# Kernel tuning notes

Measured on AMD Instinct MI355X. Metric: run time of the kernel, lower is better.

The kernel has to match this reference:

```python
import jax, jax.numpy as jnp
import numpy as np

B, N, D, H = 8, 1024, 768, 12
HD = D // H  # 64


def setup_inputs() -> dict:
    key = jax.random.key(0)
    ks = jax.random.split(key, 10)
    input_graph = jax.random.normal(ks[0], (B, N, D), dtype=jnp.float32)
    u = jax.random.uniform(ks[1], (B, N, N), dtype=jnp.float32)
    keep = jax.random.uniform(ks[2], (B, N, N)) < 0.15
    adj = jnp.where(keep, u, 0.0)
    s = 1.0 / np.sqrt(D)
    Wq = jax.random.normal(ks[3], (D, D), dtype=jnp.float32) * s
    bq = jnp.zeros((D,), dtype=jnp.float32)
    Wk = jax.random.normal(ks[4], (D, D), dtype=jnp.float32) * s
    bk = jnp.zeros((D,), dtype=jnp.float32)
    Wv = jax.random.normal(ks[5], (D, D), dtype=jnp.float32) * s
    bv = jnp.zeros((D,), dtype=jnp.float32)
    beta = jnp.asarray(0.1, dtype=jnp.float32)
    return {"input_graph": input_graph, "adj": adj, "Wq": Wq, "bq": bq,
            "Wk": Wk, "bk": bk, "Wv": Wv, "bv": bv, "beta": beta}


def _split_heads(x):
    # [B,N,D] -> [B,H,N,HD]
    b, n, _ = x.shape
    return x.reshape(b, n, H, HD).transpose(0, 2, 1, 3)


def reference(input_graph, adj, Wq, bq, Wk, bk, Wv, bv, beta):
    q = _split_heads(input_graph @ Wq + bq)  # [B,H,N,HD]
    k = _split_heads(input_graph @ Wk + bk)
    v = _split_heads(input_graph @ Wv + bv)
    scores = jnp.einsum('bhqd,bhkd->bhqk', q, k) / jnp.sqrt(jnp.asarray(HD, input_graph.dtype))
    adj_e = adj[:, None, :, :]  # [B,1,N,N]
    scores = scores + beta * adj_e
    scores = jnp.where(adj_e > 0, scores, jnp.asarray(-9e15, scores.dtype))
    probs = jax.nn.softmax(scores, axis=-1)
    out = jnp.einsum('bhqk,bhkd->bhqd', probs, v)  # [B,H,N,HD]
    return out.transpose(0, 2, 1, 3).reshape(input_graph.shape[0], input_graph.shape[1], D)
```

## Files before the change

kernel.cpp:

```cpp
#include <hip/hip_runtime.h>

#define B_ 8
#define N_ 1024
#define D_ 768
#define H_ 12
#define HD_ 64

#define LOG2E 1.4426950408889634f

typedef __attribute__((ext_vector_type(8))) short bf16x8;
typedef __attribute__((ext_vector_type(4))) short short4_t;
typedef __attribute__((ext_vector_type(4))) float f32x4;
typedef __attribute__((ext_vector_type(16))) float f32x16;
typedef unsigned int u32;

__device__ __forceinline__ short f2bf(float f) {
  union { float f; unsigned u; } v; v.f = f;
  unsigned u = v.u;
  unsigned r = u + 0x7fffu + ((u >> 16) & 1u);
  return (short)(r >> 16);
}
__device__ __forceinline__ float bf2f(short s) {
  union { unsigned u; float f; } v;
  v.u = ((unsigned)(unsigned short)s) << 16;
  return v.f;
}
__device__ __forceinline__ u32 cvtpk(float a, float b) {
  u32 r;
  asm("v_cvt_pk_bf16_f32 %0, %1, %2" : "=v"(r) : "v"(a), "v"(b));
  return r;
}
__device__ __forceinline__ void pl32swap(u32& a, u32& b) {
  asm("v_permlane32_swap_b32 %0, %1" : "+v"(a), "+v"(b));
}

__device__ __forceinline__ void gload_lds16(const void* g, void* l) {
  __builtin_amdgcn_global_load_lds((const __attribute__((address_space(1))) u32*)g,
                                   (__attribute__((address_space(3))) u32*)l, 16, 0, 0);
}

__global__ __launch_bounds__(256)
void cvt_kernel(const float* __restrict__ X, short* __restrict__ Xb,
                const float* __restrict__ Wq, const float* __restrict__ Wk,
                const float* __restrict__ Wv, short* __restrict__ Wt3) {
  const int bid = blockIdx.x;
  const int tid = threadIdx.x;

  if (bid < 3072) {
    int i = (bid * 256 + tid) * 8;
    float4 a = *(const float4*)(X + i);
    float4 b = *(const float4*)(X + i + 4);
    bf16x8 o;
    o[0] = f2bf(a.x); o[1] = f2bf(a.y); o[2] = f2bf(a.z); o[3] = f2bf(a.w);
    o[4] = f2bf(b.x); o[5] = f2bf(b.y); o[6] = f2bf(b.z); o[7] = f2bf(b.w);
    *(bf16x8*)(Xb + i) = o;
  } else {
    const int i = bid - 3072;
    const int z = i / 576;
    const int rem = i % 576;
    const int bx = rem % 24, by = rem / 24;
    const float* W = z == 0 ? Wq : (z == 1 ? Wk : Wv);
    short* O = Wt3 + (size_t)z * D_ * D_;
    __shared__ float t[32][33];
    const int n0 = bx * 32, k0 = by * 32;
    const int tx = tid & 31, ty = tid >> 5;
#pragma unroll
    for (int j = 0; j < 4; j++)
      t[ty + 8 * j][tx] = W[(size_t)(k0 + ty + 8 * j) * D_ + n0 + tx];
    __syncthreads();
#pragma unroll
    for (int j = 0; j < 4; j++)
      O[(size_t)(n0 + ty + 8 * j) * D_ + k0 + tx] = f2bf(t[tx][ty + 8 * j]);
  }
}

__global__ __launch_bounds__(256, 4)
void gemm_madj_kernel(const short* __restrict__ Xb, const short* __restrict__ Wt3,
                      const float* __restrict__ bq, const float* __restrict__ bk,
                      const float* __restrict__ bv, short* __restrict__ QKV,
                      const float* __restrict__ adj, const float* __restrict__ beta_p,
                      short* __restrict__ madjF) {
  __shared__ __align__(16) char smem[32768];
  const int bid = blockIdx.x;
  const int tid = threadIdx.x;

  if (bid < 1152) {
    const int z = bid / 384;
    const int n0 = ((bid >> 6) % 6) * 128;
    const int m0 = (bid & 63) * 128;
    const short* Wt = Wt3 + (size_t)z * D_ * D_;
    const float* bias = z == 0 ? bq : (z == 1 ? bk : bv);
    short* C = QKV + (size_t)z * (B_ * N_) * D_;
    const float alpha = (z == 0) ? 0.125f * LOG2E : 1.0f;

    const int lane = tid & 63;
    const int wid = tid >> 6;
    const int wr = (wid >> 1) * 64;
    const int wc = (wid & 1) * 64;
    const int l15 = lane & 15;
    const int lg = lane >> 4;

    short* At = (short*)smem;
    short* Bt = (short*)smem + 8192;

    f32x4 acc[4][4];
#pragma unroll
    for (int m = 0; m < 4; m++)
#pragma unroll
      for (int n = 0; n < 4; n++)
        acc[m][n] = (f32x4){0.f, 0.f, 0.f, 0.f};

    const int srow_l = lane >> 2;
    const int sc8 = (((lane & 3) ^ ((lane >> 2) & 3)) * 8);
    const short* ag = Xb + (size_t)(m0 + wid * 16 + srow_l) * D_ + sc8;
    const short* bg = Wt + (size_t)(n0 + wid * 16 + srow_l) * D_ + sc8;

    auto stage = [&](int bi, int k0) {
#pragma unroll
      for (int p = 0; p < 2; p++) {
        gload_lds16(ag + (size_t)(64 * p) * D_ + k0, At + bi * 4096 + (wid + 4 * p) * 512);
        gload_lds16(bg + (size_t)(64 * p) * D_ + k0, Bt + bi * 4096 + (wid + 4 * p) * 512);
      }
    };

    stage(0, 0);
    for (int k0 = 0; k0 < D_; k0 += 32) {
      const int cur = (k0 >> 5) & 1;
      __syncthreads();
      if (k0 + 32 < D_) stage(cur ^ 1, k0 + 32);

      bf16x8 af[4], bfr[4];
#pragma unroll
      for (int m = 0; m < 4; m++) {
        const int row = wr + m * 16 + l15;
        af[m] = *(const bf16x8*)(At + cur * 4096 + row * 32 + (lg ^ (l15 & 3)) * 8);
      }
#pragma unroll
      for (int n = 0; n < 4; n++) {
        const int row = wc + n * 16 + l15;
        bfr[n] = *(const bf16x8*)(Bt + cur * 4096 + row * 32 + (lg ^ (l15 & 3)) * 8);
      }
#pragma unroll
      for (int m = 0; m < 4; m++)
#pragma unroll
        for (int n = 0; n < 4; n++)
          acc[m][n] = __builtin_amdgcn_mfma_f32_16x16x32_bf16(af[m], bfr[n], acc[m][n], 0, 0, 0);
    }

    if (z == 2) {
#pragma unroll
      for (int n = 0; n < 4; n++) {
        const int col = n0 + wc + n * 16 + l15;
        const float bval = bias[col];
        const int hh = col >> 6, dd = col & 63;
#pragma unroll
        for (int m = 0; m < 4; m++) {
          const int row = m0 + wr + m * 16 + 4 * lg;
          const int bb = row >> 10, nn = row & 1023;
          short4_t o;
#pragma unroll
          for (int r = 0; r < 4; r++) o[r] = f2bf(acc[m][n][r] + bval);
          *(short4_t*)&C[(((size_t)bb * H_ + hh) * HD_ + dd) * N_ + nn] = o;
        }
      }
    } else {
#pragma unroll
      for (int n = 0; n < 4; n++) {
        const int col = n0 + wc + n * 16 + l15;
        const float bval = bias[col];
#pragma unroll
        for (int m = 0; m < 4; m++) {
#pragma unroll
          for (int r = 0; r < 4; r++) {
            const int row = m0 + wr + m * 16 + 4 * lg + r;
            C[(size_t)row * D_ + col] = f2bf((acc[m][n][r] + bval) * alpha);
          }
        }
      }
    }
  } else {
    const int j = bid - 1152;
    const int b = j >> 8;
    const int rr = j & 255;
    const int qt64 = rr >> 4, kt = rr & 15;
    const float b2 = beta_p[0] * LOG2E;
    const float MASKV = -9.0e15f * LOG2E;

    float* Lt = (float*)smem;
    {
      const int row = tid >> 2, cs = (tid & 3) * 16;
      const float* ap = adj + ((size_t)b * N_ + qt64 * 64 + row) * (size_t)N_ + kt * 64 + cs;
#pragma unroll
      for (int jj = 0; jj < 4; jj++)
        *(float4*)(Lt + row * 68 + cs + 4 * jj) = *(const float4*)(ap + 4 * jj);
    }
    __syncthreads();

    const int a = tid >> 1, cb = tid & 1;
    const int lane_att = a & 63;
    const int l31 = lane_att & 31, hia = lane_att >> 5;
    const int q_local = 32 * (a >> 6) + l31;

    short vals[16];
#pragma unroll
    for (int t = 0; t < 4; t++) {
      float4 a4 = *(const float4*)(Lt + q_local * 68 + 32 * cb + 8 * t + 4 * hia);
      float av[4] = {a4.x, a4.y, a4.z, a4.w};
#pragma unroll
      for (int r2 = 0; r2 < 4; r2++) {
        float av_ = av[r2];
        vals[4 * t + r2] = f2bf((av_ > 0.f) ? b2 * av_ : MASKV);
      }
    }
    short* o = madjF + ((size_t)((b * 8 + (qt64 >> 1)) * 16 + kt)) * 8192 +
               (qt64 & 1) * 4096 + tid * 16;
    bf16x8 lo, hi;
#pragma unroll
    for (int jj = 0; jj < 8; jj++) { lo[jj] = vals[jj]; hi[jj] = vals[8 + jj]; }
    *(bf16x8*)o = lo;
    *(bf16x8*)(o + 8) = hi;
  }
}

__global__ __launch_bounds__(256, 3)
void attn_kernel(const short* __restrict__ QKV, const short* __restrict__ madjF,
                 float* __restrict__ out) {
  const short* Qb = QKV;
  const short* Kb = QKV + (size_t)(B_ * N_) * D_;
  const short* VTg = QKV + 2 * (size_t)(B_ * N_) * D_;

  const int wg = blockIdx.x;
  const int b = wg & 7;
  const int rem = wg >> 3;
  const int h = rem >> 3;
  const int qt = rem & 7;

  const int tid = threadIdx.x;
  const int lane = tid & 63;
  const int w = tid >> 6;
  const int l31 = lane & 31;
  const int hi = lane >> 5;
  const int swz = lane & 7;

  const int q0 = qt * 128;
  const size_t seq0 = (size_t)b * N_;
  const int hc = h * HD_;

  __shared__ short Kt[2][64][64];
  __shared__ short VTt[2][64][64];

  bf16x8 qf[4];
  {
    const short* qp = Qb + (seq0 + q0 + 32 * w + l31) * (size_t)D_ + hc + 8 * hi;
#pragma unroll
    for (int s = 0; s < 4; s++) qf[s] = *(const bf16x8*)(qp + 16 * s);
  }

  f32x16 acc0 = {}, acc1 = {};
  float l_ = 0.f;

  const int srow = 16 * w + (lane >> 3);
  const int sc8 = ((lane & 7) ^ (lane >> 3)) * 8;
  const short* kg = Kb + (seq0 + srow) * (size_t)D_ + hc + sc8;
  const short* vg = VTg + ((size_t)(b * H_ + h) * HD_ + srow) * N_ + sc8;
  const short* mg = madjF + ((size_t)(b * 8 + qt) * 16) * 8192 + (w * 64 + lane) * 32;

  auto stage = [&](int bi, int kt) {
    const int k0 = kt * 64;
    gload_lds16(kg + (size_t)k0 * D_, ((short*)Kt[bi]) + (size_t)w * 1024);
    gload_lds16(kg + (size_t)(k0 + 8) * D_, ((short*)Kt[bi]) + (size_t)w * 1024 + 512);
    gload_lds16(vg + k0, ((short*)VTt[bi]) + (size_t)w * 1024);
    gload_lds16(vg + k0 + 8 * (size_t)N_, ((short*)VTt[bi]) + (size_t)w * 1024 + 512);
  };

  stage(0, 0);
  bf16x8 mj[4];
#pragma unroll
  for (int j = 0; j < 4; j++) mj[j] = *(const bf16x8*)(mg + 8 * j);

  for (int kt = 0; kt < 16; kt++) {
    const int cur = kt & 1;
    __syncthreads();
    if (kt < 15) stage(cur ^ 1, kt + 1);
    const int ktn = kt < 15 ? kt + 1 : 15;
    bf16x8 mjn[4];
#pragma unroll
    for (int j = 0; j < 4; j++) mjn[j] = *(const bf16x8*)(mg + (size_t)ktn * 8192 + 8 * j);

    f32x16 sA0, sA1;
    {
      f32x16 c;
#pragma unroll
      for (int r = 0; r < 16; r++) c[r] = bf2f(mj[r >> 3][r & 7]);
#pragma unroll
      for (int s = 0; s < 4; s++) {
        bf16x8 kf = *(const bf16x8*)&Kt[cur][l31][((2 * s + hi) ^ swz) * 8];
        c = __builtin_amdgcn_mfma_f32_32x32x16_bf16(kf, qf[s], c, 0, 0, 0);
      }
      sA0 = c;
    }
    {
      f32x16 c;
#pragma unroll
      for (int r = 0; r < 16; r++) c[r] = bf2f(mj[2 + (r >> 3)][r & 7]);
#pragma unroll
      for (int s = 0; s < 4; s++) {
        bf16x8 kf = *(const bf16x8*)&Kt[cur][32 + l31][((2 * s + hi) ^ swz) * 8];
        c = __builtin_amdgcn_mfma_f32_32x32x16_bf16(kf, qf[s], c, 0, 0, 0);
      }
      sA1 = c;
    }
#pragma unroll
    for (int j = 0; j < 4; j++) mj[j] = mjn[j];

    float ps = 0.f;
    u32 fw[16];
    {
#pragma unroll
      for (int r = 0; r < 16; r++) { sA0[r] = __builtin_exp2f(sA0[r]); ps += sA0[r]; }
#pragma unroll
      for (int r = 0; r < 16; r++) { sA1[r] = __builtin_exp2f(sA1[r]); ps += sA1[r]; }
      u32 w0[8], w1[8];
#pragma unroll
      for (int c = 0; c < 8; c++) w0[c] = cvtpk(sA0[2 * c], sA0[2 * c + 1]);
#pragma unroll
      for (int c = 0; c < 8; c++) w1[c] = cvtpk(sA1[2 * c], sA1[2 * c + 1]);
      pl32swap(w0[0], w0[2]); fw[0] = w0[0];  fw[2] = w0[2];
      pl32swap(w0[1], w0[3]); fw[1] = w0[1];  fw[3] = w0[3];
      pl32swap(w0[4], w0[6]); fw[4] = w0[4];  fw[6] = w0[6];
      pl32swap(w0[5], w0[7]); fw[5] = w0[5];  fw[7] = w0[7];
      pl32swap(w1[0], w1[2]); fw[8] = w1[0];  fw[10] = w1[2];
      pl32swap(w1[1], w1[3]); fw[9] = w1[1];  fw[11] = w1[3];
      pl32swap(w1[4], w1[6]); fw[12] = w1[4]; fw[14] = w1[6];
      pl32swap(w1[5], w1[7]); fw[13] = w1[5]; fw[15] = w1[7];
    }
    ps += __shfl_xor(ps, 32);
    l_ += ps;

#pragma unroll
    for (int ks = 0; ks < 4; ks++) {
      union { u32 u[4]; bf16x8 v; } pu;
      pu.u[0] = fw[4 * ks]; pu.u[1] = fw[4 * ks + 1];
      pu.u[2] = fw[4 * ks + 2]; pu.u[3] = fw[4 * ks + 3];
      bf16x8 vf0 = *(const bf16x8*)&VTt[cur][l31][((2 * ks + hi) ^ swz) * 8];
      bf16x8 vf1 = *(const bf16x8*)&VTt[cur][32 + l31][((2 * ks + hi) ^ swz) * 8];
      acc0 = __builtin_amdgcn_mfma_f32_32x32x16_bf16(vf0, pu.v, acc0, 0, 0, 0);
      acc1 = __builtin_amdgcn_mfma_f32_32x32x16_bf16(vf1, pu.v, acc1, 0, 0, 0);
    }
  }

  const float invl = 1.f / l_;
  float* orow = out + (seq0 + q0 + 32 * w + l31) * (size_t)D_ + hc;
#pragma unroll
  for (int t = 0; t < 4; t++) {
    float4 o0, o1;
    o0.x = acc0[4 * t] * invl;     o0.y = acc0[4 * t + 1] * invl;
    o0.z = acc0[4 * t + 2] * invl; o0.w = acc0[4 * t + 3] * invl;
    o1.x = acc1[4 * t] * invl;     o1.y = acc1[4 * t + 1] * invl;
    o1.z = acc1[4 * t + 2] * invl; o1.w = acc1[4 * t + 3] * invl;
    *(float4*)(orow + 8 * t + 4 * hi) = o0;
    *(float4*)(orow + 8 * t + 4 * hi + 32) = o1;
  }
}

extern "C" void kernel_launch(void* const* d_in, const int* in_sizes, int n_in,
                              void* d_out, int out_size, void* d_ws, size_t ws_size,
                              hipStream_t stream) {
  const float* X    = (const float*)d_in[0];
  const float* adj  = (const float*)d_in[1];
  const float* Wq   = (const float*)d_in[2];
  const float* bq   = (const float*)d_in[3];
  const float* Wk   = (const float*)d_in[4];
  const float* bk   = (const float*)d_in[5];
  const float* Wv   = (const float*)d_in[6];
  const float* bv   = (const float*)d_in[7];
  const float* beta = (const float*)d_in[8];
  float* out = (float*)d_out;

  short* Xb    = (short*)d_ws;
  short* Wt3   = Xb + (size_t)(B_ * N_) * D_;
  short* QKV   = Wt3 + 3 * (size_t)D_ * D_;
  short* madjF = QKV + 3 * (size_t)(B_ * N_) * D_;

  cvt_kernel<<<dim3(4800), 256, 0, stream>>>(X, Xb, Wq, Wk, Wv, Wt3);
  gemm_madj_kernel<<<dim3(3200), 256, 0, stream>>>(Xb, Wt3, bq, bk, bv, QKV, adj, beta, madjF);
  attn_kernel<<<dim3(768), 256, 0, stream>>>(QKV, madjF, out);
}
```

Baseline: 108.8 us.

## Software-pipeline QK of next tile with softmax-PV of previous tile

Restructures the attention main loop so the QK^T MFMAs for tile t+1 are issued before the exp/pack/PV work for tile t, unrolled by two with ping-pong score registers. V tiles get a triple LDS buffer so the V tile for t-1 stays resident while t+1 is being loaded. The aim is to overlap transcendental and pack work with matrix-core work and hide latency. It costs extra registers for a second set of score accumulators and more LDS, which may lower occupancy.

```diff
diff --git a/kernel.cpp b/kernel.cpp
--- a/kernel.cpp
+++ b/kernel.cpp
@@ -247,7 +247,7 @@
   const int hc = h * HD_;
 
   __shared__ short Kt[2][64][64];
-  __shared__ short VTt[2][64][64];
+  __shared__ short VTt[3][64][64];
 
   bf16x8 qf[4];
   {
@@ -265,89 +265,107 @@
   const short* vg = VTg + ((size_t)(b * H_ + h) * HD_ + srow) * N_ + sc8;
   const short* mg = madjF + ((size_t)(b * 8 + qt) * 16) * 8192 + (w * 64 + lane) * 32;
 
-  auto stage = [&](int bi, int kt) {
+  auto stageK = [&](int bi, int kt) {
     const int k0 = kt * 64;
     gload_lds16(kg + (size_t)k0 * D_, ((short*)Kt[bi]) + (size_t)w * 1024);
     gload_lds16(kg + (size_t)(k0 + 8) * D_, ((short*)Kt[bi]) + (size_t)w * 1024 + 512);
+  };
+  auto stageV = [&](int bi, int kt) {
+    const int k0 = kt * 64;
     gload_lds16(vg + k0, ((short*)VTt[bi]) + (size_t)w * 1024);
     gload_lds16(vg + k0 + 8 * (size_t)N_, ((short*)VTt[bi]) + (size_t)w * 1024 + 512);
   };
 
-  stage(0, 0);
-  bf16x8 mj[4];
-#pragma unroll
-  for (int j = 0; j < 4; j++) mj[j] = *(const bf16x8*)(mg + 8 * j);
-
-  for (int kt = 0; kt < 16; kt++) {
-    const int cur = kt & 1;
-    __syncthreads();
-    if (kt < 15) stage(cur ^ 1, kt + 1);
-    const int ktn = kt < 15 ? kt + 1 : 15;
-    bf16x8 mjn[4];
-#pragma unroll
-    for (int j = 0; j < 4; j++) mjn[j] = *(const bf16x8*)(mg + (size_t)ktn * 8192 + 8 * j);
-
-    f32x16 sA0, sA1;
-    {
-      f32x16 c;
-#pragma unroll
-      for (int r = 0; r < 16; r++) c[r] = bf2f(mj[r >> 3][r & 7]);
-#pragma unroll
-      for (int s = 0; s < 4; s++) {
-        bf16x8 kf = *(const bf16x8*)&Kt[cur][l31][((2 * s + hi) ^ swz) * 8];
-        c = __builtin_amdgcn_mfma_f32_32x32x16_bf16(kf, qf[s], c, 0, 0, 0);
-      }
-      sA0 = c;
-    }
-    {
-      f32x16 c;
-#pragma unroll
-      for (int r = 0; r < 16; r++) c[r] = bf2f(mj[2 + (r >> 3)][r & 7]);
-#pragma unroll
-      for (int s = 0; s < 4; s++) {
-        bf16x8 kf = *(const bf16x8*)&Kt[cur][32 + l31][((2 * s + hi) ^ swz) * 8];
-        c = __builtin_amdgcn_mfma_f32_32x32x16_bf16(kf, qf[s], c, 0, 0, 0);
-      }
-      sA1 = c;
-    }
-#pragma unroll
-    for (int j = 0; j < 4; j++) mj[j] = mjn[j];
-
+  auto QK = [&](int kbuf, const bf16x8* mj, f32x16& s0, f32x16& s1) {
+    const short* K0 = (const short*)Kt[kbuf];
+    f32x16 c;
+#pragma unroll
+    for (int r = 0; r < 16; r++) c[r] = bf2f(mj[r >> 3][r & 7]);
+#pragma unroll
+    for (int s = 0; s < 4; s++) {
+      bf16x8 kf = *(const bf16x8*)(K0 + l31 * 64 + (((2 * s + hi) ^ swz) * 8));
+      c = __builtin_amdgcn_mfma_f32_32x32x16_bf16(kf, qf[s], c, 0, 0, 0);
+    }
+    s0 = c;
+#pragma unroll
+    for (int r = 0; r < 16; r++) c[r] = bf2f(mj[2 + (r >> 3)][r & 7]);
+#pragma unroll
+    for (int s = 0; s < 4; s++) {
+      bf16x8 kf = *(const bf16x8*)(K0 + (32 + l31) * 64 + (((2 * s + hi) ^ swz) * 8));
+      c = __builtin_amdgcn_mfma_f32_32x32x16_bf16(kf, qf[s], c, 0, 0, 0);
+    }
+    s1 = c;
+  };
+
+  auto PACKPV = [&](f32x16& s0, f32x16& s1, int vbuf) {
     float ps = 0.f;
     u32 fw[16];
-    {
-#pragma unroll
-      for (int r = 0; r < 16; r++) { sA0[r] = __builtin_exp2f(sA0[r]); ps += sA0[r]; }
-#pragma unroll
-      for (int r = 0; r < 16; r++) { sA1[r] = __builtin_exp2f(sA1[r]); ps += sA1[r]; }
-      u32 w0[8], w1[8];
-#pragma unroll
-      for (int c = 0; c < 8; c++) w0[c] = cvtpk(sA0[2 * c], sA0[2 * c + 1]);
-#pragma unroll
-      for (int c = 0; c < 8; c++) w1[c] = cvtpk(sA1[2 * c], sA1[2 * c + 1]);
-      pl32swap(w0[0], w0[2]); fw[0] = w0[0];  fw[2] = w0[2];
-      pl32swap(w0[1], w0[3]); fw[1] = w0[1];  fw[3] = w0[3];
-      pl32swap(w0[4], w0[6]); fw[4] = w0[4];  fw[6] = w0[6];
-      pl32swap(w0[5], w0[7]); fw[5] = w0[5];  fw[7] = w0[7];
-      pl32swap(w1[0], w1[2]); fw[8] = w1[0];  fw[10] = w1[2];
-      pl32swap(w1[1], w1[3]); fw[9] = w1[1];  fw[11] = w1[3];
-      pl32swap(w1[4], w1[6]); fw[12] = w1[4]; fw[14] = w1[6];
-      pl32swap(w1[5], w1[7]); fw[13] = w1[5]; fw[15] = w1[7];
-    }
+#pragma unroll
+    for (int r = 0; r < 16; r++) { s0[r] = __builtin_exp2f(s0[r]); ps += s0[r]; }
+#pragma unroll
+    for (int r = 0; r < 16; r++) { s1[r] = __builtin_exp2f(s1[r]); ps += s1[r]; }
+    u32 w0[8], w1[8];
+#pragma unroll
+    for (int c = 0; c < 8; c++) w0[c] = cvtpk(s0[2 * c], s0[2 * c + 1]);
+#pragma unroll
+    for (int c = 0; c < 8; c++) w1[c] = cvtpk(s1[2 * c], s1[2 * c + 1]);
+    pl32swap(w0[0], w0[2]); fw[0] = w0[0];  fw[2] = w0[2];
+    pl32swap(w0[1], w0[3]); fw[1] = w0[1];  fw[3] = w0[3];
+    pl32swap(w0[4], w0[6]); fw[4] = w0[4];  fw[6] = w0[6];
+    pl32swap(w0[5], w0[7]); fw[5] = w0[5];  fw[7] = w0[7];
+    pl32swap(w1[0], w1[2]); fw[8] = w1[0];  fw[10] = w1[2];
+    pl32swap(w1[1], w1[3]); fw[9] = w1[1];  fw[11] = w1[3];
+    pl32swap(w1[4], w1[6]); fw[12] = w1[4]; fw[14] = w1[6];
+    pl32swap(w1[5], w1[7]); fw[13] = w1[5]; fw[15] = w1[7];
     ps += __shfl_xor(ps, 32);
     l_ += ps;
-
+    const short* V0 = (const short*)VTt[vbuf];
 #pragma unroll
     for (int ks = 0; ks < 4; ks++) {
       union { u32 u[4]; bf16x8 v; } pu;
       pu.u[0] = fw[4 * ks]; pu.u[1] = fw[4 * ks + 1];
       pu.u[2] = fw[4 * ks + 2]; pu.u[3] = fw[4 * ks + 3];
-      bf16x8 vf0 = *(const bf16x8*)&VTt[cur][l31][((2 * ks + hi) ^ swz) * 8];
-      bf16x8 vf1 = *(const bf16x8*)&VTt[cur][32 + l31][((2 * ks + hi) ^ swz) * 8];
+      bf16x8 vf0 = *(const bf16x8*)(V0 + l31 * 64 + (((2 * ks + hi) ^ swz) * 8));
+      bf16x8 vf1 = *(const bf16x8*)(V0 + (32 + l31) * 64 + (((2 * ks + hi) ^ swz) * 8));
       acc0 = __builtin_amdgcn_mfma_f32_32x32x16_bf16(vf0, pu.v, acc0, 0, 0, 0);
       acc1 = __builtin_amdgcn_mfma_f32_32x32x16_bf16(vf1, pu.v, acc1, 0, 0, 0);
     }
+  };
+
+  bf16x8 mjc[4], mjn[4];
+  f32x16 sE0, sE1, sO0, sO1;
+
+  stageK(0, 0); stageV(0, 0);
+#pragma unroll
+  for (int j = 0; j < 4; j++) mjc[j] = *(const bf16x8*)(mg + 8 * j);
+  __syncthreads();
+  stageK(1, 1); stageV(1, 1);
+#pragma unroll
+  for (int j = 0; j < 4; j++) mjn[j] = *(const bf16x8*)(mg + 8192 + 8 * j);
+  QK(0, mjc, sE0, sE1);
+
+  for (int tp = 0; tp < 7; tp++) {
+    const int t0 = 2 * tp + 1, t1 = 2 * tp + 2;
+    __syncthreads();
+    stageK((t0 + 1) & 1, t0 + 1);
+    stageV((t0 + 1) % 3, t0 + 1);
+#pragma unroll
+    for (int j = 0; j < 4; j++) mjc[j] = *(const bf16x8*)(mg + (size_t)(t0 + 1) * 8192 + 8 * j);
+    QK(t0 & 1, mjn, sO0, sO1);
+    PACKPV(sE0, sE1, (t0 - 1) % 3);
+    __syncthreads();
+    stageK((t1 + 1) & 1, t1 + 1);
+    stageV((t1 + 1) % 3, t1 + 1);
+#pragma unroll
+    for (int j = 0; j < 4; j++) mjn[j] = *(const bf16x8*)(mg + (size_t)(t1 + 1) * 8192 + 8 * j);
+    QK(t1 & 1, mjc, sE0, sE1);
+    PACKPV(sO0, sO1, (t1 - 1) % 3);
   }
+
+  __syncthreads();
+  QK(1, mjn, sO0, sO1);
+  PACKPV(sE0, sE1, 14 % 3);
+  PACKPV(sO0, sO1, 15 % 3);
 
   const float invl = 1.f / l_;
   float* orow = out + (seq0 + q0 + 32 * w + l31) * (size_t)D_ + hc;
```

After: 119.3 us. +9.7%, slower.

## Software-pipeline QK softmax with previous tile's PV using triple-buffered V

Applied to the files above, without the earlier changes.

Restructures the attention loop so the PV MFMAs for tile t-1 are interleaved with the QK MFMAs and exp/pack work for tile t. V now uses a three-slot LDS ring, because the previous tile's V must stay resident while the next one is staged. The cross-lane row-sum reduction moves out of the loop and runs once at the end. This is meant to hide the latency of exp and packing behind matrix work, at the cost of more registers (two packed P buffers) and more LDS, which may lower occupancy.

```diff
diff --git a/kernel.cpp b/kernel.cpp
--- a/kernel.cpp
+++ b/kernel.cpp
@@ -222,6 +222,44 @@
   }
 }
 
+#define QK_HALF(SREG, K0, ROWOFF, MJA, MJB)                                    \
+  {                                                                            \
+    f32x16 c_;                                                                 \
+    _Pragma("unroll") for (int r_ = 0; r_ < 8; r_++) c_[r_] = bf2f(MJA[r_]);   \
+    _Pragma("unroll") for (int r_ = 0; r_ < 8; r_++) c_[8 + r_] = bf2f(MJB[r_]);\
+    _Pragma("unroll") for (int s_ = 0; s_ < 4; s_++) {                         \
+      bf16x8 kf_ = *(const bf16x8*)((K0) + ((ROWOFF) + l31) * 64 +             \
+                                    (((2 * s_ + hi) ^ swz) * 8));              \
+      c_ = __builtin_amdgcn_mfma_f32_32x32x16_bf16(kf_, qf[s_], c_, 0, 0, 0);  \
+    }                                                                          \
+    SREG = c_;                                                                 \
+  }
+
+#define PACK_HALF(SREG, FW, OFF)                                               \
+  {                                                                            \
+    _Pragma("unroll") for (int r_ = 0; r_ < 16; r_++) {                        \
+      SREG[r_] = __builtin_exp2f(SREG[r_]); ps += SREG[r_];                    \
+    }                                                                          \
+    u32 wv_[8];                                                                \
+    _Pragma("unroll") for (int c_ = 0; c_ < 8; c_++)                           \
+      wv_[c_] = cvtpk(SREG[2 * c_], SREG[2 * c_ + 1]);                         \
+    pl32swap(wv_[0], wv_[2]); FW[(OFF) + 0] = wv_[0]; FW[(OFF) + 2] = wv_[2];  \
+    pl32swap(wv_[1], wv_[3]); FW[(OFF) + 1] = wv_[1]; FW[(OFF) + 3] = wv_[3];  \
+    pl32swap(wv_[4], wv_[6]); FW[(OFF) + 4] = wv_[4]; FW[(OFF) + 6] = wv_[6];  \
+    pl32swap(wv_[5], wv_[7]); FW[(OFF) + 5] = wv_[5]; FW[(OFF) + 7] = wv_[7];  \
+  }
+
+#define PV_HALF(FW, V0, KS0)                                                   \
+  _Pragma("unroll") for (int ks_ = (KS0); ks_ < (KS0) + 2; ks_++) {            \
+    union { u32 u[4]; bf16x8 v; } pu_;                                         \
+    pu_.u[0] = FW[4 * ks_];     pu_.u[1] = FW[4 * ks_ + 1];                    \
+    pu_.u[2] = FW[4 * ks_ + 2]; pu_.u[3] = FW[4 * ks_ + 3];                    \
+    bf16x8 vf0_ = *(const bf16x8*)((V0) + l31 * 64 + (((2 * ks_ + hi) ^ swz) * 8)); \
+    bf16x8 vf1_ = *(const bf16x8*)((V0) + (32 + l31) * 64 + (((2 * ks_ + hi) ^ swz) * 8)); \
+    acc0 = __builtin_amdgcn_mfma_f32_32x32x16_bf16(vf0_, pu_.v, acc0, 0, 0, 0);\
+    acc1 = __builtin_amdgcn_mfma_f32_32x32x16_bf16(vf1_, pu_.v, acc1, 0, 0, 0);\
+  }
+
 __global__ __launch_bounds__(256, 3)
 void attn_kernel(const short* __restrict__ QKV, const short* __restrict__ madjF,
                  float* __restrict__ out) {
@@ -247,7 +285,7 @@
   const int hc = h * HD_;
 
   __shared__ short Kt[2][64][64];
-  __shared__ short VTt[2][64][64];
+  __shared__ short VTt[3][64][64];
 
   bf16x8 qf[4];
   {
@@ -265,90 +303,79 @@
   const short* vg = VTg + ((size_t)(b * H_ + h) * HD_ + srow) * N_ + sc8;
   const short* mg = madjF + ((size_t)(b * 8 + qt) * 16) * 8192 + (w * 64 + lane) * 32;
 
-  auto stage = [&](int bi, int kt) {
-    const int k0 = kt * 64;
-    gload_lds16(kg + (size_t)k0 * D_, ((short*)Kt[bi]) + (size_t)w * 1024);
-    gload_lds16(kg + (size_t)(k0 + 8) * D_, ((short*)Kt[bi]) + (size_t)w * 1024 + 512);
-    gload_lds16(vg + k0, ((short*)VTt[bi]) + (size_t)w * 1024);
-    gload_lds16(vg + k0 + 8 * (size_t)N_, ((short*)VTt[bi]) + (size_t)w * 1024 + 512);
-  };
-
-  stage(0, 0);
-  bf16x8 mj[4];
-#pragma unroll
-  for (int j = 0; j < 4; j++) mj[j] = *(const bf16x8*)(mg + 8 * j);
-
-  for (int kt = 0; kt < 16; kt++) {
-    const int cur = kt & 1;
+  bf16x8 mjc[4], mjn[4];
+  u32 fwP[16], fwN[16];
+
+  {
+    gload_lds16(kg, ((short*)Kt[0]) + (size_t)w * 1024);
+    gload_lds16(kg + 8 * (size_t)D_, ((short*)Kt[0]) + (size_t)w * 1024 + 512);
+    gload_lds16(vg, ((short*)VTt[0]) + (size_t)w * 1024);
+    gload_lds16(vg + 8 * (size_t)N_, ((short*)VTt[0]) + (size_t)w * 1024 + 512);
+#pragma unroll
+    for (int j = 0; j < 4; j++) mjc[j] = *(const bf16x8*)(mg + 8 * j);
     __syncthreads();
-    if (kt < 15) stage(cur ^ 1, kt + 1);
-    const int ktn = kt < 15 ? kt + 1 : 15;
-    bf16x8 mjn[4];
-#pragma unroll
-    for (int j = 0; j < 4; j++) mjn[j] = *(const bf16x8*)(mg + (size_t)ktn * 8192 + 8 * j);
-
-    f32x16 sA0, sA1;
-    {
-      f32x16 c;
-#pragma unroll
-      for (int r = 0; r < 16; r++) c[r] = bf2f(mj[r >> 3][r & 7]);
-#pragma unroll
-      for (int s = 0; s < 4; s++) {
-        bf16x8 kf = *(const bf16x8*)&Kt[cur][l31][((2 * s + hi) ^ swz) * 8];
-        c = __builtin_amdgcn_mfma_f32_32x32x16_bf16(kf, qf[s], c, 0, 0, 0);
-      }
-      sA0 = c;
+    gload_lds16(kg + (size_t)64 * D_, ((short*)Kt[1]) + (size_t)w * 1024);
+    gload_lds16(kg + (size_t)72 * D_, ((short*)Kt[1]) + (size_t)w * 1024 + 512);
+    gload_lds16(vg + 64, ((short*)VTt[1]) + (size_t)w * 1024);
+    gload_lds16(vg + 64 + 8 * (size_t)N_, ((short*)VTt[1]) + (size_t)w * 1024 + 512);
+#pragma unroll
+    for (int j = 0; j < 4; j++) mjn[j] = *(const bf16x8*)(mg + 8192 + 8 * j);
+
+    float ps = 0.f;
+    f32x16 s0, s1;
+    const short* K0 = (const short*)Kt[0];
+    QK_HALF(s0, K0, 0, mjc[0], mjc[1]);
+    PACK_HALF(s0, fwP, 0);
+    QK_HALF(s1, K0, 32, mjc[2], mjc[3]);
+    PACK_HALF(s1, fwP, 8);
+    l_ += ps;
+#pragma unroll
+    for (int j = 0; j < 4; j++) mjc[j] = mjn[j];
+  }
+
+  int vprev = 0;
+  int vstage = 2;
+  for (int t = 1; t < 16; t++) {
+    __syncthreads();
+    if (t < 15) {
+      const int k0 = (t + 1) * 64;
+      gload_lds16(kg + (size_t)k0 * D_, ((short*)Kt[(t + 1) & 1]) + (size_t)w * 1024);
+      gload_lds16(kg + (size_t)(k0 + 8) * D_, ((short*)Kt[(t + 1) & 1]) + (size_t)w * 1024 + 512);
+      gload_lds16(vg + k0, ((short*)VTt[vstage]) + (size_t)w * 1024);
+      gload_lds16(vg + k0 + 8 * (size_t)N_, ((short*)VTt[vstage]) + (size_t)w * 1024 + 512);
+#pragma unroll
+      for (int j = 0; j < 4; j++)
+        mjn[j] = *(const bf16x8*)(mg + (size_t)(t + 1) * 8192 + 8 * j);
     }
-    {
-      f32x16 c;
-#pragma unroll
-      for (int r = 0; r < 16; r++) c[r] = bf2f(mj[2 + (r >> 3)][r & 7]);
-#pragma unroll
-      for (int s = 0; s < 4; s++) {
-        bf16x8 kf = *(const bf16x8*)&Kt[cur][32 + l31][((2 * s + hi) ^ swz) * 8];
-        c = __builtin_amdgcn_mfma_f32_32x32x16_bf16(kf, qf[s], c, 0, 0, 0);
-      }
-      sA1 = c;
-    }
-#pragma unroll
-    for (int j = 0; j < 4; j++) mj[j] = mjn[j];
-
+
+    const short* K0 = (const short*)Kt[t & 1];
+    const short* V0 = (const short*)VTt[vprev];
     float ps = 0.f;
-    u32 fw[16];
-    {
-#pragma unroll
-      for (int r = 0; r < 16; r++) { sA0[r] = __builtin_exp2f(sA0[r]); ps += sA0[r]; }
-#pragma unroll
-      for (int r = 0; r < 16; r++) { sA1[r] = __builtin_exp2f(sA1[r]); ps += sA1[r]; }
-      u32 w0[8], w1[8];
-#pragma unroll
-      for (int c = 0; c < 8; c++) w0[c] = cvtpk(sA0[2 * c], sA0[2 * c + 1]);
-#pragma unroll
-      for (int c = 0; c < 8; c++) w1[c] = cvtpk(sA1[2 * c], sA1[2 * c + 1]);
-      pl32swap(w0[0], w0[2]); fw[0] = w0[0];  fw[2] = w0[2];
-      pl32swap(w0[1], w0[3]); fw[1] = w0[1];  fw[3] = w0[3];
-      pl32swap(w0[4], w0[6]); fw[4] = w0[4];  fw[6] = w0[6];
-      pl32swap(w0[5], w0[7]); fw[5] = w0[5];  fw[7] = w0[7];
-      pl32swap(w1[0], w1[2]); fw[8] = w1[0];  fw[10] = w1[2];
-      pl32swap(w1[1], w1[3]); fw[9] = w1[1];  fw[11] = w1[3];
-      pl32swap(w1[4], w1[6]); fw[12] = w1[4]; fw[14] = w1[6];
-      pl32swap(w1[5], w1[7]); fw[13] = w1[5]; fw[15] = w1[7];
-    }
-    ps += __shfl_xor(ps, 32);
+    f32x16 s0, s1;
+
+    QK_HALF(s0, K0, 0, mjc[0], mjc[1]);
+    PV_HALF(fwP, V0, 0);
+    PACK_HALF(s0, fwN, 0);
+    QK_HALF(s1, K0, 32, mjc[2], mjc[3]);
+    PV_HALF(fwP, V0, 2);
+    PACK_HALF(s1, fwN, 8);
     l_ += ps;
 
 #pragma unroll
-    for (int ks = 0; ks < 4; ks++) {
-      union { u32 u[4]; bf16x8 v; } pu;
-      pu.u[0] = fw[4 * ks]; pu.u[1] = fw[4 * ks + 1];
-      pu.u[2] = fw[4 * ks + 2]; pu.u[3] = fw[4 * ks + 3];
-      bf16x8 vf0 = *(const bf16x8*)&VTt[cur][l31][((2 * ks + hi) ^ swz) * 8];
-      bf16x8 vf1 = *(const bf16x8*)&VTt[cur][32 + l31][((2 * ks + hi) ^ swz) * 8];
-      acc0 = __builtin_amdgcn_mfma_f32_32x32x16_bf16(vf0, pu.v, acc0, 0, 0, 0);
-      acc1 = __builtin_amdgcn_mfma_f32_32x32x16_bf16(vf1, pu.v, acc1, 0, 0, 0);
-    }
-  }
-
+    for (int i = 0; i < 16; i++) fwP[i] = fwN[i];
+#pragma unroll
+    for (int j = 0; j < 4; j++) mjc[j] = mjn[j];
+    vprev = (vprev == 2) ? 0 : vprev + 1;
+    vstage = (vstage == 2) ? 0 : vstage + 1;
+  }
+
+  {
+    const short* V0 = (const short*)VTt[vprev];
+    PV_HALF(fwP, V0, 0);
+    PV_HALF(fwP, V0, 2);
+  }
+
+  l_ += __shfl_xor(l_, 32);
   const float invl = 1.f / l_;
   float* orow = out + (seq0 + q0 + 32 * w + l31) * (size_t)D_ + hc;
 #pragma unroll
```

New measurement: 108.4 us (median of 3 runs). Within noise of the previous version (-0.3%).
